# Kernel tuning notes

Measured on AMD Instinct MI355X. Metric: run time of the kernel, lower is better.

The kernel has to match this reference:

```python
import jax, jax.numpy as jnp
import numpy as np

NUM_HEADS = 16
EPS = 1e-8


def _dyn_quant(x):
    # per-token symmetric int8 quantization (dynamic input scale)
    s = jnp.maximum(jnp.max(jnp.abs(x), axis=-1, keepdims=True) / 127.0, EPS)
    q = jnp.clip(jnp.round(x / s), -127.0, 127.0)
    return q, s


def _quant_weight(w):
    # per-output-channel symmetric int8 weight quantization; w: [out, in]
    s = jnp.maximum(jnp.max(jnp.abs(w), axis=1, keepdims=True) / 127.0, EPS)
    q = jnp.clip(jnp.round(w / s), -127.0, 127.0)
    return q, s


def _w8a8_linear(x, w, b):
    # W8A8 GEMM with int32-exact accumulation (values fit exactly in fp32),
    # dequantized by per-token input scale * per-channel weight scale.
    qx, sx = _dyn_quant(x)          # [B,N,C], [B,N,1]
    qw, sw = _quant_weight(w)       # [O,C],   [O,1]
    y = jnp.einsum('bnc,oc->bno', qx, qw) * (sx * sw[:, 0])
    return y + b


def setup_inputs() -> dict:
    key = jax.random.key(0)
    ks = jax.random.split(key, 9)
    B, N, L, C = 2, 4096, 512, 2048
    sc = 0.02  # realistic weight init scale
    return {
        'x':    jax.random.normal(ks[0], (B, N, C), jnp.float32),
        'cond': jax.random.normal(ks[1], (B, L, C), jnp.float32),
        'mask': jnp.zeros((B, N, L), jnp.float32),  # additive attention mask
        'wq': jax.random.normal(ks[2], (C, C), jnp.float32) * sc,
        'bq': jnp.zeros((C,), jnp.float32),
        'wk': jax.random.normal(ks[3], (C, C), jnp.float32) * sc,
        'bk': jnp.zeros((C,), jnp.float32),
        'wv': jax.random.normal(ks[4], (C, C), jnp.float32) * sc,
        'bv': jnp.zeros((C,), jnp.float32),
        'wo': jax.random.normal(ks[5], (C, C), jnp.float32) * sc,
        'bo': jnp.zeros((C,), jnp.float32),
    }


def reference(x, cond, mask, wq, bq, wk, bk, wv, bv, wo, bo):
    B, N, C = x.shape
    L = cond.shape[1]
    H = NUM_HEADS
    D = C // H
    inv_sqrt_d = np.float32(1.0 / np.sqrt(D))

    # quantized Q projection, fp K/V projections
    q = _w8a8_linear(x, wq, bq).reshape(B, N, H, D).transpose(0, 2, 1, 3)      # [B,H,N,D]
    k = (cond @ wk.T + bk).reshape(B, L, H, D).transpose(0, 2, 1, 3)           # [B,H,L,D]
    v = (cond @ wv.T + bv).reshape(B, L, H, D).transpose(0, 2, 1, 3)           # [B,H,L,D]

    # SDPA cross-attention with additive mask broadcast over heads
    scores = jnp.einsum('bhnd,bhld->bhnl', q, k) * inv_sqrt_d + mask[:, None]
    attn = jax.nn.softmax(scores, axis=-1)
    o = jnp.einsum('bhnl,bhld->bhnd', attn, v)
    o = o.transpose(0, 2, 1, 3).reshape(B, N, C)

    # fused quant_sum (per-token requant) + quantized output projection
    return _w8a8_linear(o, wo, bo)
```

## Files before the change

kernel.cpp:

```cpp
#include <hip/hip_runtime.h>
#include <cstdint>
#include <cstddef>


typedef __bf16 bf16;
typedef __bf16 bf16x8 __attribute__((ext_vector_type(8)));
typedef __bf16 bf16x4 __attribute__((ext_vector_type(4)));
typedef float  f32x4  __attribute__((ext_vector_type(4)));
typedef int    i32x4  __attribute__((ext_vector_type(4)));

#define DEV __device__ __forceinline__

static constexpr int CB = 2;
static constexpr int CN = 4096;
static constexpr int CL = 512;
static constexpr int CC = 2048;
static constexpr int CH = 16;
static constexpr int CD = 128;
static constexpr int TOK = CB * CN;
static constexpr int LR  = CB * CL;

DEV void gl_lds16(const void* g, void* l) {
  __builtin_amdgcn_global_load_lds(
      (const __attribute__((address_space(1))) unsigned int*)g,
      (__attribute__((address_space(3))) unsigned int*)l, 16, 0, 0);
}

DEV f32x4 mfma16(bf16x8 a, bf16x8 b, f32x4 c) {
  return __builtin_amdgcn_mfma_f32_16x16x32_bf16(a, b, c, 0, 0, 0);
}

DEV i32x4 mfma_i8(i32x4 a, i32x4 b, i32x4 c) {
  return __builtin_amdgcn_mfma_i32_16x16x64_i8(a, b, c, 0, 0, 0);
}

DEV void quant_row_body(const float* __restrict__ in, signed char* __restrict__ q,
                        float* __restrict__ scale, const int r, const int t)
{
  const float* x = in + (size_t)r * CC;
  const float4 v0 = ((const float4*)x)[2 * t];
  const float4 v1 = ((const float4*)x)[2 * t + 1];
  float m = fmaxf(fmaxf(fmaxf(fabsf(v0.x), fabsf(v0.y)), fmaxf(fabsf(v0.z), fabsf(v0.w))),
                  fmaxf(fmaxf(fabsf(v1.x), fabsf(v1.y)), fmaxf(fabsf(v1.z), fabsf(v1.w))));
#pragma unroll
  for (int off = 32; off > 0; off >>= 1) m = fmaxf(m, __shfl_xor(m, off));
  __shared__ float sm[4];
  if ((t & 63) == 0) sm[t >> 6] = m;
  __syncthreads();
  m = fmaxf(fmaxf(sm[0], sm[1]), fmaxf(sm[2], sm[3]));
  const float s = fmaxf(m / 127.0f, 1e-8f);
  if (t == 0) scale[r] = s;
  const float a[8] = {v0.x, v0.y, v0.z, v0.w, v1.x, v1.y, v1.z, v1.w};
  int2 pk;
  int lo = 0, hi = 0;
#pragma unroll
  for (int j = 0; j < 4; j++) {
    const int b0 = (int)fminf(fmaxf(rintf(a[j]     / s), -127.f), 127.f);
    const int b1 = (int)fminf(fmaxf(rintf(a[4 + j] / s), -127.f), 127.f);
    lo |= (b0 & 255) << (8 * j);
    hi |= (b1 & 255) << (8 * j);
  }
  pk.x = lo; pk.y = hi;
  const int c0 = t * 8;
  const int f = (r >> 1) & 3;
  const int pos = (c0 & ~63) | ((((c0 >> 4) & 3) ^ f) << 4) | (c0 & 15);
  *(int2*)&q[(size_t)r * CC + pos] = pk;
}

__global__ __launch_bounds__(256) void quant_rows_i8(
    const float* __restrict__ in, signed char* __restrict__ q,
    float* __restrict__ scale)
{
  quant_row_body(in, q, scale, blockIdx.x, threadIdx.x);
}

__global__ __launch_bounds__(256) void quant_w2(
    const float* __restrict__ wq, const float* __restrict__ wo,
    signed char* __restrict__ qwq, signed char* __restrict__ qwo,
    float* __restrict__ swq, float* __restrict__ swo)
{
  int r = blockIdx.x;
  if (r < CC) quant_row_body(wq, qwq, swq, r, threadIdx.x);
  else        quant_row_body(wo, qwo, swo, r - CC, threadIdx.x);
}

__global__ __launch_bounds__(256) void split3_k(
    const float* __restrict__ cond, const float* __restrict__ wk,
    const float* __restrict__ wv,
    bf16* __restrict__ ch,  bf16* __restrict__ cl_,
    bf16* __restrict__ wkh, bf16* __restrict__ wkl,
    bf16* __restrict__ wvh, bf16* __restrict__ wvl)
{
  const int NC = (LR * CC / 4) / 256;
  const int NW = (CC * CC / 4) / 256;
  int blk = blockIdx.x;
  const float* in; bf16* hi; bf16* lo;
  if (blk < NC)           { in = cond; hi = ch;  lo = cl_; }
  else if (blk < NC + NW) { blk -= NC;      in = wk; hi = wkh; lo = wkl; }
  else                    { blk -= NC + NW; in = wv; hi = wvh; lo = wvl; }
  const size_t i = (size_t)blk * 256 + threadIdx.x;
  const float4 v = ((const float4*)in)[i];
  const float a[4] = {v.x, v.y, v.z, v.w};
  bf16x4 h4, l4;
#pragma unroll
  for (int j = 0; j < 4; j++) {
    bf16 h = (bf16)a[j];
    h4[j] = h;
    l4[j] = (bf16)(a[j] - (float)h);
  }
  ((bf16x4*)hi)[i] = h4;
  ((bf16x4*)lo)[i] = l4;
}

template <int MODE>
__global__ __launch_bounds__(256) void gemm_i8(
    const signed char* __restrict__ A, const signed char* __restrict__ B,
    float* __restrict__ out0, bf16* __restrict__ outH, bf16* __restrict__ outL,
    const float* __restrict__ rowS, const float* __restrict__ colS,
    const float* __restrict__ bias, const int Nd, const int K)
{
  __shared__ signed char sA[2][128 * 64] __attribute__((aligned(16)));
  __shared__ signed char sB[2][128 * 64] __attribute__((aligned(16)));
  const int t = threadIdx.x;
  int lin = blockIdx.y * 16 + blockIdx.x;
  lin = (lin & 7) * 128 + (lin >> 3);
  const int m0 = (lin >> 4) * 128, n0 = (lin & 15) * 128;
  const int srow = t >> 2, scol = (t & 3) * 16;
  const signed char* aP = A + (size_t)(m0 + srow) * K + scol;
  const signed char* bP = B + (size_t)(n0 + srow) * K + scol;
  const int lane = t & 63, wave = t >> 6;
  const int wm = (wave >> 1) * 64, wn = (wave & 1) * 64;
  const int quad = lane >> 4, l16 = lane & 15;
  i32x4 acc[4][4] = {};

  gl_lds16(aP,                  &sA[0][t * 16]);
  gl_lds16(aP + (size_t)64 * K, &sA[0][4096 + t * 16]);
  gl_lds16(bP,                  &sB[0][t * 16]);
  gl_lds16(bP + (size_t)64 * K, &sB[0][4096 + t * 16]);
  __syncthreads();

  int cur = 0;
  for (int kb = 0; kb < K; kb += 64) {
    const int nx = kb + 64;
    if (nx < K) {
      gl_lds16(aP + nx,                  &sA[cur ^ 1][t * 16]);
      gl_lds16(aP + nx + (size_t)64 * K, &sA[cur ^ 1][4096 + t * 16]);
      gl_lds16(bP + nx,                  &sB[cur ^ 1][t * 16]);
      gl_lds16(bP + nx + (size_t)64 * K, &sB[cur ^ 1][4096 + t * 16]);
    }
    i32x4 fa[4], fb[4];
#pragma unroll
    for (int i = 0; i < 4; i++) {
      const int ra = wm + i * 16 + l16;
      const int rb = wn + i * 16 + l16;
      fa[i] = *(const i32x4*)&sA[cur][ra * 64 + (quad ^ ((ra >> 1) & 3)) * 16];
      fb[i] = *(const i32x4*)&sB[cur][rb * 64 + (quad ^ ((rb >> 1) & 3)) * 16];
    }
#pragma unroll
    for (int mt = 0; mt < 4; mt++)
#pragma unroll
      for (int nt = 0; nt < 4; nt++)
        acc[mt][nt] = mfma_i8(fa[mt], fb[nt], acc[mt][nt]);
    __syncthreads();
    cur ^= 1;
  }

#pragma unroll
  for (int mt = 0; mt < 4; mt++)
#pragma unroll
    for (int nt = 0; nt < 4; nt++)
#pragma unroll
      for (int rg = 0; rg < 4; rg++) {
        const int mr = m0 + wm + mt * 16 + quad * 4 + rg;
        const int nc = n0 + wn + nt * 16 + l16;
        const float a = (float)acc[mt][nt][rg];
        const float sc = rowS[mr] * colS[nc];
        const float v = a * sc + bias[nc];
        if (MODE == 0) {
          out0[(size_t)mr * Nd + nc] = v;
        } else {
          const bf16 h = (bf16)v;
          outH[(size_t)mr * Nd + nc] = h;
          outL[(size_t)mr * Nd + nc] = (bf16)(v - (float)h);
        }
      }
}

__global__ __launch_bounds__(256) void gemm_kv2(
    const bf16* __restrict__ Ah, const bf16* __restrict__ Al,
    const bf16* __restrict__ B0h, const bf16* __restrict__ B0l,
    const bf16* __restrict__ B1h, const bf16* __restrict__ B1l,
    bf16* __restrict__ outKh, bf16* __restrict__ outKl,
    bf16* __restrict__ outVh, bf16* __restrict__ outVl,
    const float* __restrict__ bk, const float* __restrict__ bv)
{
  __shared__ char arena[128 * 129 * 4] __attribute__((aligned(16)));
  bf16 (*sAh)[4096] = (bf16 (*)[4096])(arena);
  bf16 (*sBh)[4096] = (bf16 (*)[4096])(arena + 16384);
  bf16 (*sAl)[4096] = (bf16 (*)[4096])(arena + 32768);
  bf16 (*sBl)[4096] = (bf16 (*)[4096])(arena + 49152);
  const int t = threadIdx.x;
  const int K = CC;
  int lin = (blockIdx.z * 8 + blockIdx.y) * 16 + blockIdx.x;
  lin = (lin & 7) * 32 + (lin >> 3);
  const int n0 = (lin & 15) * 128;
  const int m0 = ((lin >> 4) & 7) * 128;
  const int kv = lin >> 7;
  const bf16* Bh = kv ? B1h : B0h;
  const bf16* Bl = kv ? B1l : B0l;
  const int srow = t >> 2, c8 = t & 3, scol = c8 * 8;
  const int r1 = srow + 64;
  const int d0 = srow * 32 + ((c8 ^ ((srow >> 1) & 3)) * 8);
  const int d1 = r1   * 32 + ((c8 ^ ((r1   >> 1) & 3)) * 8);
  const bf16* aP  = Ah + (size_t)(m0 + srow) * K + scol;
  const bf16* bP  = Bh + (size_t)(n0 + srow) * K + scol;
  const bf16* aPl = Al + (size_t)(m0 + srow) * K + scol;
  const bf16* bPl = Bl + (size_t)(n0 + srow) * K + scol;
  const int lane = t & 63, wave = t >> 6;
  const int wm = (wave >> 1) * 64, wn = (wave & 1) * 64;
  const int quad = lane >> 4, l16 = lane & 15;
  f32x4 acc[4][4] = {};

  uint4 g0, g1, g2, g3, g4, g5, g6, g7;
#define KV_LOAD(kb)                                                 \
  do {                                                              \
    g0 = *(const uint4*)(aP  + (kb));                               \
    g1 = *(const uint4*)(aP  + (kb) + (size_t)64 * K);              \
    g2 = *(const uint4*)(bP  + (kb));                               \
    g3 = *(const uint4*)(bP  + (kb) + (size_t)64 * K);              \
    g4 = *(const uint4*)(aPl + (kb));                               \
    g5 = *(const uint4*)(aPl + (kb) + (size_t)64 * K);              \
    g6 = *(const uint4*)(bPl + (kb));                               \
    g7 = *(const uint4*)(bPl + (kb) + (size_t)64 * K);              \
  } while (0)
#define KV_WRITE(buf)                                               \
  do {                                                              \
    *(uint4*)&sAh[buf][d0] = g0;  *(uint4*)&sAh[buf][d1] = g1;      \
    *(uint4*)&sBh[buf][d0] = g2;  *(uint4*)&sBh[buf][d1] = g3;      \
    *(uint4*)&sAl[buf][d0] = g4;  *(uint4*)&sAl[buf][d1] = g5;      \
    *(uint4*)&sBl[buf][d0] = g6;  *(uint4*)&sBl[buf][d1] = g7;      \
  } while (0)

  KV_LOAD(0);
  KV_WRITE(0);
  KV_LOAD(32);

  const int NS = K / 32;
  for (int ci = 0; ci < NS; ci++) {
    const int cur = ci & 1;
    __syncthreads();
    if (ci + 1 < NS) KV_WRITE(cur ^ 1);
    if (ci + 2 < NS) KV_LOAD((ci + 2) * 32);
    bf16x8 fa[4], fb[4], fal[4], fbl[4];
#pragma unroll
    for (int i = 0; i < 4; i++) {
      const int ra = wm + i * 16 + l16;
      const int rb = wn + i * 16 + l16;
      const int oa = ra * 32 + ((quad ^ ((ra >> 1) & 3)) * 8);
      const int ob = rb * 32 + ((quad ^ ((rb >> 1) & 3)) * 8);
      fa[i]  = *(const bf16x8*)&sAh[cur][oa];
      fb[i]  = *(const bf16x8*)&sBh[cur][ob];
      fal[i] = *(const bf16x8*)&sAl[cur][oa];
      fbl[i] = *(const bf16x8*)&sBl[cur][ob];
    }
#pragma unroll
    for (int mt = 0; mt < 4; mt++)
#pragma unroll
      for (int nt = 0; nt < 4; nt++) {
        f32x4 c = acc[mt][nt];
        c = mfma16(fa[mt],  fb[nt],  c);
        c = mfma16(fa[mt],  fbl[nt], c);
        c = mfma16(fal[mt], fb[nt],  c);
        acc[mt][nt] = c;
      }
  }
#undef KV_LOAD
#undef KV_WRITE

  if (kv == 0) {
#pragma unroll
    for (int mt = 0; mt < 4; mt++)
#pragma unroll
      for (int nt = 0; nt < 4; nt++)
#pragma unroll
        for (int rg = 0; rg < 4; rg++) {
          const int mr = m0 + wm + mt * 16 + quad * 4 + rg;
          const int nc = n0 + wn + nt * 16 + l16;
          const float v = acc[mt][nt][rg] + bk[nc];
          const bf16 h = (bf16)v;
          outKh[(size_t)mr * CC + nc] = h;
          outKl[(size_t)mr * CC + nc] = (bf16)(v - (float)h);
        }
  } else {
    __syncthreads();
    float (*tile)[129] = (float (*)[129])arena;
#pragma unroll
    for (int mt = 0; mt < 4; mt++)
#pragma unroll
      for (int nt = 0; nt < 4; nt++)
#pragma unroll
        for (int rg = 0; rg < 4; rg++) {
          const int lm = wm + mt * 16 + quad * 4 + rg;
          const int ln = wn + nt * 16 + l16;
          tile[lm][ln] = acc[mt][nt][rg] + bv[n0 + ln];
        }
    __syncthreads();
    const int h = n0 >> 7, b = m0 >> 9, lbase = m0 & (CL - 1);
    const int d = t & 127, half = t >> 7;
    const size_t orow = ((size_t)(b * CH + h) * CD + d) * CL + lbase + half * 64;
#pragma unroll
    for (int jv = 0; jv < 8; jv++) {
      bf16x8 h8, l8;
#pragma unroll
      for (int j = 0; j < 8; j++) {
        const float v = tile[half * 64 + jv * 8 + j][d];
        const bf16 hh = (bf16)v;
        h8[j] = hh;
        l8[j] = (bf16)(v - (float)hh);
      }
      *(bf16x8*)&outVh[orow + jv * 8] = h8;
      *(bf16x8*)&outVl[orow + jv * 8] = l8;
    }
  }
}

__global__ __launch_bounds__(1024, 4) void attn_k(
    const bf16* __restrict__ qh, const bf16* __restrict__ ql,
    const bf16* __restrict__ kh, const bf16* __restrict__ kl,
    const bf16* __restrict__ vth, const bf16* __restrict__ vtl,
    const float* __restrict__ mask, float* __restrict__ O)
{
  __shared__ char arena[34816 + 32768 + 36864] __attribute__((aligned(16)));
  bf16 (*ksb)[2][32][136] = (bf16 (*)[2][32][136])arena;
  bf16 (*vtb)[2][128][32] = (bf16 (*)[2][128][32])(arena + 34816);
  float (*ps)[16][36] = (float (*)[16][36])(arena + 34816 + 32768);
  const int t = threadIdx.x, lane = t & 63, w = t >> 6;
  const int quad = lane >> 4, l16 = lane & 15;
  int lin = (blockIdx.z * 16 + blockIdx.y) * 16 + blockIdx.x;
  lin = (lin & 7) * 64 + (lin >> 3);
  const int n0 = (lin & 15) * 256;
  const int h  = (lin >> 4) & 15;
  const int b  = lin >> 8;
  const int bh = b * CH + h;
  const size_t qrow0 = (size_t)b * CN + n0;
  const float* mrow_base = mask + ((size_t)b * CN + n0 + w * 16 + quad * 4) * CL;

  const int pl   = t >> 9;
  const int krow = (t >> 4) & 31, ksg = t & 15;
  const int vrow = (t >> 2) & 127, vsg = t & 3;
  const bf16* kPsrc = pl ? kl : kh;
  const bf16* vPsrc = pl ? vtl : vth;
  const int vc = (vsg ^ ((vrow >> 3) & 3)) * 8;
  uint4 kr, vr;
  kr = *(const uint4*)(kPsrc + ((size_t)b * CL + krow) * CC + h * CD + ksg * 8);
  vr = *(const uint4*)(vPsrc + ((size_t)bh * CD + vrow) * CL + vsg * 8);

  bf16x8 qfh[4], qfl[4];
  {
    bf16* qs = (bf16*)arena;
    const int row = t >> 2, sg = t & 3;
    {
      const bf16* src = qh + (qrow0 + row) * CC + h * CD + sg * 32;
      bf16* dst = qs + row * 136 + sg * 32;
#pragma unroll
      for (int j = 0; j < 4; j++) ((uint4*)dst)[j] = ((const uint4*)src)[j];
    }
    __syncthreads();
#pragma unroll
    for (int s = 0; s < 4; s++)
      qfh[s] = *(const bf16x8*)&qs[(w * 16 + l16) * 136 + s * 32 + quad * 8];
    __syncthreads();
    {
      const bf16* src = ql + (qrow0 + row) * CC + h * CD + sg * 32;
      bf16* dst = qs + row * 136 + sg * 32;
#pragma unroll
      for (int j = 0; j < 4; j++) ((uint4*)dst)[j] = ((const uint4*)src)[j];
    }
    __syncthreads();
#pragma unroll
    for (int s = 0; s < 4; s++)
      qfl[s] = *(const bf16x8*)&qs[(w * 16 + l16) * 136 + s * 32 + quad * 8];
    __syncthreads();
  }

  *(uint4*)&ksb[0][pl][krow][ksg * 8] = kr;
  *(uint4*)&vtb[0][pl][vrow][vc] = vr;
  kr = *(const uint4*)(kPsrc + ((size_t)b * CL + 32 + krow) * CC + h * CD + ksg * 8);
  vr = *(const uint4*)(vPsrc + ((size_t)bh * CD + vrow) * CL + 32 + vsg * 8);

  f32x4 oacc[8] = {};
  f32x4 suma = {};
  const bf16 one = (bf16)1.0f;
  const bf16x8 ones = {one, one, one, one, one, one, one, one};
  const float isd = 0.08838834764831845f;

  for (int ci = 0; ci < CL / 32; ci++) {
    const int cur = ci & 1;
    __syncthreads();
    if (ci + 1 < CL / 32) {
      *(uint4*)&ksb[cur ^ 1][pl][krow][ksg * 8] = kr;
      *(uint4*)&vtb[cur ^ 1][pl][vrow][vc] = vr;
    }
    if (ci + 2 < CL / 32) {
      const int lcn = (ci + 2) * 32;
      kr = *(const uint4*)(kPsrc + ((size_t)b * CL + lcn + krow) * CC + h * CD + ksg * 8);
      vr = *(const uint4*)(vPsrc + ((size_t)bh * CD + vrow) * CL + lcn + vsg * 8);
    }
    const int lc = ci * 32;
    float mcur[2][4];
#pragma unroll
    for (int rg = 0; rg < 4; rg++) {
      const float* mrp = mrow_base + (size_t)rg * CL + lc;
      mcur[0][rg] = mrp[l16];
      mcur[1][rg] = mrp[16 + l16];
    }

    f32x4 sacc[2] = {};
    __builtin_amdgcn_s_setprio(1);
#pragma unroll
    for (int s = 0; s < 4; s++) {
#pragma unroll
      for (int lt = 0; lt < 2; lt++) {
        bf16x8 kbh = *(const bf16x8*)&ksb[cur][0][lt * 16 + l16][s * 32 + quad * 8];
        bf16x8 kbl = *(const bf16x8*)&ksb[cur][1][lt * 16 + l16][s * 32 + quad * 8];
        sacc[lt] = mfma16(qfh[s], kbh, sacc[lt]);
        sacc[lt] = mfma16(qfh[s], kbl, sacc[lt]);
        sacc[lt] = mfma16(qfl[s], kbh, sacc[lt]);
      }
    }
    __builtin_amdgcn_s_setprio(0);

    float u[2][4];
#pragma unroll
    for (int rg = 0; rg < 4; rg++) {
      u[0][rg] = __expf(sacc[0][rg] * isd + mcur[0][rg]);
      u[1][rg] = __expf(sacc[1][rg] * isd + mcur[1][rg]);
    }

#pragma unroll
    for (int lt = 0; lt < 2; lt++)
#pragma unroll
      for (int rg = 0; rg < 4; rg++)
        ps[w][quad * 4 + rg][lt * 16 + l16] = u[lt][rg];
    const float4 p0 = *(const float4*)&ps[w][l16][quad * 8];
    const float4 p1 = *(const float4*)&ps[w][l16][quad * 8 + 4];
    const float pv[8] = {p0.x, p0.y, p0.z, p0.w, p1.x, p1.y, p1.z, p1.w};
    bf16x8 ph, plv;
#pragma unroll
    for (int j = 0; j < 8; j++) {
      bf16 hh = (bf16)pv[j];
      ph[j] = hh;
      plv[j] = (bf16)(pv[j] - (float)hh);
    }

    suma = mfma16(ph, ones, suma);
    suma = mfma16(plv, ones, suma);
    __builtin_amdgcn_s_setprio(1);
#pragma unroll
    for (int nt = 0; nt < 8; nt++) {
      const int vrr = nt * 16 + l16;
      const int vsw = (quad ^ ((vrr >> 3) & 3)) * 8;
      bf16x8 vbh = *(const bf16x8*)&vtb[cur][0][vrr][vsw];
      bf16x8 vbl = *(const bf16x8*)&vtb[cur][1][vrr][vsw];
      f32x4 c = oacc[nt];
      c = mfma16(ph, vbh, c);
      c = mfma16(ph, vbl, c);
      c = mfma16(plv, vbh, c);
      oacc[nt] = c;
    }
    __builtin_amdgcn_s_setprio(0);
  }

  f32x4 inv;
#pragma unroll
  for (int rg = 0; rg < 4; rg++) inv[rg] = 1.0f / suma[rg];
#pragma unroll
  for (int nt = 0; nt < 8; nt++)
#pragma unroll
    for (int rg = 0; rg < 4; rg++) {
      const size_t row = qrow0 + w * 16 + quad * 4 + rg;
      O[row * CC + h * CD + nt * 16 + l16] = oacc[nt][rg] * inv[rg];
    }
}

extern "C" void kernel_launch(void* const* d_in, const int* in_sizes, int n_in,
                              void* d_out, int out_size, void* d_ws, size_t ws_size,
                              hipStream_t stream)
{
  (void)in_sizes; (void)n_in; (void)out_size; (void)ws_size;
  const float* x    = (const float*)d_in[0];
  const float* cond = (const float*)d_in[1];
  const float* mask = (const float*)d_in[2];
  const float* wq   = (const float*)d_in[3];
  const float* bq   = (const float*)d_in[4];
  const float* wk   = (const float*)d_in[5];
  const float* bk   = (const float*)d_in[6];
  const float* wv   = (const float*)d_in[7];
  const float* bv   = (const float*)d_in[8];
  const float* wo   = (const float*)d_in[9];
  const float* bo   = (const float*)d_in[10];
  float* out = (float*)d_out;

  char* wsb = (char*)d_ws;
  size_t off = 0;
  auto alloc = [&](size_t bytes) -> char* {
    char* p = wsb + off;
    off += (bytes + 255) & ~(size_t)255;
    return p;
  };
  signed char* qx  = (signed char*)alloc((size_t)TOK * CC);
  signed char* qwq = (signed char*)alloc((size_t)CC * CC);
  bf16* ch  = (bf16*)alloc((size_t)LR * CC * 2);
  bf16* cl_ = (bf16*)alloc((size_t)LR * CC * 2);
  bf16* wkh = (bf16*)alloc((size_t)CC * CC * 2);
  bf16* wkl = (bf16*)alloc((size_t)CC * CC * 2);
  bf16* wvh = (bf16*)alloc((size_t)CC * CC * 2);
  bf16* wvl = (bf16*)alloc((size_t)CC * CC * 2);
  (void)alloc((size_t)16 << 20);
  float* Obuf = (float*)qx;
  bf16* qhb = (bf16*)alloc((size_t)TOK * CC * 2);
  bf16* qlb = (bf16*)alloc((size_t)TOK * CC * 2);
  bf16* khb = (bf16*)alloc((size_t)LR * CC * 2);
  bf16* klb = (bf16*)alloc((size_t)LR * CC * 2);
  bf16* vth = (bf16*)alloc((size_t)LR * CC * 2);
  bf16* vtl = (bf16*)alloc((size_t)LR * CC * 2);
  signed char* qwo = (signed char*)alloc((size_t)CC * CC);
  float* sx  = (float*)alloc((size_t)TOK * 4);
  float* swq = (float*)alloc((size_t)CC * 4);
  float* swo = (float*)alloc((size_t)CC * 4);
  float* sO  = (float*)alloc((size_t)TOK * 4);
  signed char* qO = (signed char*)qhb;

  quant_w2<<<2 * CC, 256, 0, stream>>>(wq, wo, qwq, qwo, swq, swo);
  quant_rows_i8<<<TOK, 256, 0, stream>>>(x, qx, sx);
  split3_k<<<(LR * CC / 4) / 256 + 2 * ((CC * CC / 4) / 256), 256, 0, stream>>>(
      cond, wk, wv, ch, cl_, wkh, wkl, wvh, wvl);
  gemm_i8<1><<<dim3(CC / 128, TOK / 128, 1), 256, 0, stream>>>(
      qx, qwq, nullptr, qhb, qlb, sx, swq, bq, CC, CC);
  gemm_kv2<<<dim3(CC / 128, LR / 128, 2), 256, 0, stream>>>(
      ch, cl_, wkh, wkl, wvh, wvl, khb, klb, vth, vtl, bk, bv);
  attn_k<<<dim3(CN / 256, CH, CB), 1024, 0, stream>>>(
      qhb, qlb, khb, klb, vth, vtl, mask, Obuf);
  quant_rows_i8<<<TOK, 256, 0, stream>>>(Obuf, qO, sO);
  gemm_i8<0><<<dim3(CC / 128, TOK / 128, 1), 256, 0, stream>>>(
      qO, qwo, out, nullptr, nullptr, sO, swo, bo, CC, CC);
}
```

Measured before the change: 491.0 us.

## Merge prep kernels and register-stage int8 GEMM loads with single barrier

Merges the three preprocessing launches (weight quant, input quant, bf16 hi/lo split) into one prep kernel to cut launch overhead and tail gaps. The int8 GEMM replaces direct global-to-LDS loads with register-staged loads prefetched two k-steps ahead. It also cuts the main loop to one barrier per iteration and adds a min-blocks-per-CU launch bound of 4. This adds register pressure and extra VGPR-to-LDS store instructions in exchange for hiding global load latency.

```diff
diff --git a/kernel.cpp b/kernel.cpp
--- a/kernel.cpp
+++ b/kernel.cpp
@@ -19,12 +19,6 @@
 static constexpr int CD = 128;
 static constexpr int TOK = CB * CN;
 static constexpr int LR  = CB * CL;
-
-DEV void gl_lds16(const void* g, void* l) {
-  __builtin_amdgcn_global_load_lds(
-      (const __attribute__((address_space(1))) unsigned int*)g,
-      (__attribute__((address_space(3))) unsigned int*)l, 16, 0, 0);
-}
 
 DEV f32x4 mfma16(bf16x8 a, bf16x8 b, f32x4 c) {
   return __builtin_amdgcn_mfma_f32_16x16x32_bf16(a, b, c, 0, 0, 0);
@@ -74,31 +68,10 @@
   quant_row_body(in, q, scale, blockIdx.x, threadIdx.x);
 }
 
-__global__ __launch_bounds__(256) void quant_w2(
-    const float* __restrict__ wq, const float* __restrict__ wo,
-    signed char* __restrict__ qwq, signed char* __restrict__ qwo,
-    float* __restrict__ swq, float* __restrict__ swo)
-{
-  int r = blockIdx.x;
-  if (r < CC) quant_row_body(wq, qwq, swq, r, threadIdx.x);
-  else        quant_row_body(wo, qwo, swo, r - CC, threadIdx.x);
-}
-
-__global__ __launch_bounds__(256) void split3_k(
-    const float* __restrict__ cond, const float* __restrict__ wk,
-    const float* __restrict__ wv,
-    bf16* __restrict__ ch,  bf16* __restrict__ cl_,
-    bf16* __restrict__ wkh, bf16* __restrict__ wkl,
-    bf16* __restrict__ wvh, bf16* __restrict__ wvl)
-{
-  const int NC = (LR * CC / 4) / 256;
-  const int NW = (CC * CC / 4) / 256;
-  int blk = blockIdx.x;
-  const float* in; bf16* hi; bf16* lo;
-  if (blk < NC)           { in = cond; hi = ch;  lo = cl_; }
-  else if (blk < NC + NW) { blk -= NC;      in = wk; hi = wkh; lo = wkl; }
-  else                    { blk -= NC + NW; in = wv; hi = wvh; lo = wvl; }
-  const size_t i = (size_t)blk * 256 + threadIdx.x;
+DEV void split_body(const float* __restrict__ in, bf16* __restrict__ hi,
+                    bf16* __restrict__ lo, const int blk, const int t)
+{
+  const size_t i = (size_t)blk * 256 + t;
   const float4 v = ((const float4*)in)[i];
   const float a[4] = {v.x, v.y, v.z, v.w};
   bf16x4 h4, l4;
@@ -112,8 +85,36 @@
   ((bf16x4*)lo)[i] = l4;
 }
 
+__global__ __launch_bounds__(256) void prep_k(
+    const float* __restrict__ x,  const float* __restrict__ wq,
+    const float* __restrict__ wo, const float* __restrict__ cond,
+    const float* __restrict__ wk, const float* __restrict__ wv,
+    signed char* __restrict__ qx, signed char* __restrict__ qwq,
+    signed char* __restrict__ qwo,
+    float* __restrict__ sx, float* __restrict__ swq, float* __restrict__ swo,
+    bf16* __restrict__ ch,  bf16* __restrict__ cl_,
+    bf16* __restrict__ wkh, bf16* __restrict__ wkl,
+    bf16* __restrict__ wvh, bf16* __restrict__ wvl)
+{
+  const int t = threadIdx.x;
+  const int NC = (LR * CC / 4) / 256;
+  const int NW = (CC * CC / 4) / 256;
+  int blk = blockIdx.x;
+  if (blk < TOK)        { quant_row_body(x,  qx,  sx,  blk, t); return; }
+  blk -= TOK;
+  if (blk < CC)         { quant_row_body(wq, qwq, swq, blk, t); return; }
+  blk -= CC;
+  if (blk < CC)         { quant_row_body(wo, qwo, swo, blk, t); return; }
+  blk -= CC;
+  if (blk < NC)         { split_body(cond, ch,  cl_, blk, t); return; }
+  blk -= NC;
+  if (blk < NW)         { split_body(wk,   wkh, wkl, blk, t); return; }
+  blk -= NW;
+  split_body(wv, wvh, wvl, blk, t);
+}
+
 template <int MODE>
-__global__ __launch_bounds__(256) void gemm_i8(
+__global__ __launch_bounds__(256, 4) void gemm_i8(
     const signed char* __restrict__ A, const signed char* __restrict__ B,
     float* __restrict__ out0, bf16* __restrict__ outH, bf16* __restrict__ outL,
     const float* __restrict__ rowS, const float* __restrict__ colS,
@@ -133,21 +134,32 @@
   const int quad = lane >> 4, l16 = lane & 15;
   i32x4 acc[4][4] = {};
 
-  gl_lds16(aP,                  &sA[0][t * 16]);
-  gl_lds16(aP + (size_t)64 * K, &sA[0][4096 + t * 16]);
-  gl_lds16(bP,                  &sB[0][t * 16]);
-  gl_lds16(bP + (size_t)64 * K, &sB[0][4096 + t * 16]);
-  __syncthreads();
-
-  int cur = 0;
-  for (int kb = 0; kb < K; kb += 64) {
-    const int nx = kb + 64;
-    if (nx < K) {
-      gl_lds16(aP + nx,                  &sA[cur ^ 1][t * 16]);
-      gl_lds16(aP + nx + (size_t)64 * K, &sA[cur ^ 1][4096 + t * 16]);
-      gl_lds16(bP + nx,                  &sB[cur ^ 1][t * 16]);
-      gl_lds16(bP + nx + (size_t)64 * K, &sB[cur ^ 1][4096 + t * 16]);
-    }
+  uint4 ga0, ga1, gb0, gb1;
+#define I8_LOAD(kb)                                          \
+  do {                                                       \
+    ga0 = *(const uint4*)(aP + (kb));                        \
+    ga1 = *(const uint4*)(aP + (kb) + (size_t)64 * K);       \
+    gb0 = *(const uint4*)(bP + (kb));                        \
+    gb1 = *(const uint4*)(bP + (kb) + (size_t)64 * K);       \
+  } while (0)
+#define I8_WRITE(buf)                                        \
+  do {                                                       \
+    *(uint4*)&sA[buf][t * 16]        = ga0;                  \
+    *(uint4*)&sA[buf][4096 + t * 16] = ga1;                  \
+    *(uint4*)&sB[buf][t * 16]        = gb0;                  \
+    *(uint4*)&sB[buf][4096 + t * 16] = gb1;                  \
+  } while (0)
+
+  I8_LOAD(0);
+  I8_WRITE(0);
+  I8_LOAD(64);
+
+  const int NS = K / 64;
+  for (int ci = 0; ci < NS; ci++) {
+    const int cur = ci & 1;
+    __syncthreads();
+    if (ci + 1 < NS) I8_WRITE(cur ^ 1);
+    if (ci + 2 < NS) I8_LOAD((ci + 2) * 64);
     i32x4 fa[4], fb[4];
 #pragma unroll
     for (int i = 0; i < 4; i++) {
@@ -161,9 +173,9 @@
 #pragma unroll
       for (int nt = 0; nt < 4; nt++)
         acc[mt][nt] = mfma_i8(fa[mt], fb[nt], acc[mt][nt]);
-    __syncthreads();
-    cur ^= 1;
-  }
+  }
+#undef I8_LOAD
+#undef I8_WRITE
 
 #pragma unroll
   for (int mt = 0; mt < 4; mt++)
@@ -531,10 +543,11 @@
   float* sO  = (float*)alloc((size_t)TOK * 4);
   signed char* qO = (signed char*)qhb;
 
-  quant_w2<<<2 * CC, 256, 0, stream>>>(wq, wo, qwq, qwo, swq, swo);
-  quant_rows_i8<<<TOK, 256, 0, stream>>>(x, qx, sx);
-  split3_k<<<(LR * CC / 4) / 256 + 2 * ((CC * CC / 4) / 256), 256, 0, stream>>>(
-      cond, wk, wv, ch, cl_, wkh, wkl, wvh, wvl);
+  const int NC = (LR * CC / 4) / 256;
+  const int NW = (CC * CC / 4) / 256;
+  prep_k<<<TOK + 2 * CC + NC + 2 * NW, 256, 0, stream>>>(
+      x, wq, wo, cond, wk, wv, qx, qwq, qwo, sx, swq, swo,
+      ch, cl_, wkh, wkl, wvh, wvl);
   gemm_i8<1><<<dim3(CC / 128, TOK / 128, 1), 256, 0, stream>>>(
       qx, qwq, nullptr, qhb, qlb, sx, swq, bq, CC, CC);
   gemm_kv2<<<dim3(CC / 128, LR / 128, 2), 256, 0, stream>>>(
```

Result: faster. 471.2 us (-4.0%).
